# Kernel optimization log

Hardware: AMD Instinct MI355X
Metric: run time of the kernel (lower is better)

## Reference

```python
import jax, jax.numpy as jnp
import numpy as np

B, T, D, HD, HN, O = 32, 512, 512, 64, 16, 512
EPS = 1e-5


def setup_inputs() -> dict:
    key = jax.random.key(0)
    ks = jax.random.split(key, 12)
    s = lambda fan_in: 1.0 / np.sqrt(fan_in)
    inp = {
        "inputs": jax.random.normal(ks[0], (B, T, D), dtype=jnp.float32),
        "Wq": jax.random.uniform(ks[1], (HN, D, HD), jnp.float32, -s(D), s(D)),
        "bq": jnp.zeros((HN, HD), jnp.float32),
        "Wk": jax.random.uniform(ks[2], (HN, D, HD), jnp.float32, -s(D), s(D)),
        "bk": jnp.zeros((HN, HD), jnp.float32),
        "Wv": jax.random.uniform(ks[3], (HN, D, HD), jnp.float32, -s(D), s(D)),
        "bv": jnp.zeros((HN, HD), jnp.float32),
        "Wr": jax.random.uniform(ks[4], (D, O), jnp.float32, -s(D), s(D)),
        "br": jnp.zeros((O,), jnp.float32),
        "Wo": jax.random.uniform(ks[5], (HN * HD, O), jnp.float32, -s(HN * HD), s(HN * HD)),
        "bo": jnp.zeros((O,), jnp.float32),
        "ln1_w": jnp.ones((O,), jnp.float32),
        "ln1_b": jnp.zeros((O,), jnp.float32),
        "Wfc": jax.random.uniform(ks[6], (O, O), jnp.float32, -s(O), s(O)),
        "bfc": jnp.zeros((O,), jnp.float32),
        "ln2_w": jnp.ones((O,), jnp.float32),
        "ln2_b": jnp.zeros((O,), jnp.float32),
    }
    return inp


def _layernorm(x, w, b):
    mu = jnp.mean(x, axis=-1, keepdims=True)
    var = jnp.mean(jnp.square(x - mu), axis=-1, keepdims=True)
    return (x - mu) * jax.lax.rsqrt(var + EPS) * w + b


def reference(inputs, Wq, bq, Wk, bk, Wv, bv, Wr, br, Wo, bo,
              ln1_w, ln1_b, Wfc, bfc, ln2_w, ln2_b):
    # causal mask: multiply-then-subtract as in the original
    score_mask = jnp.tril(jnp.ones((T, T), jnp.float32))        # [T,T]
    padding_mask = (score_mask == 0).astype(jnp.float32) * 1e9  # [T,T]

    residual = inputs @ Wr + br                                  # [B,T,O]

    # batched per-head projections with nonstandard activations
    q = jax.nn.relu(jnp.einsum('btd,hdf->bhtf', inputs, Wq) + bq[None, :, None, :])
    k = jax.nn.relu(jnp.einsum('btd,hdf->bhtf', inputs, Wk) + bk[None, :, None, :])
    v = jnp.tanh(jnp.einsum('btd,hdf->bhtf', inputs, Wv) + bv[None, :, None, :])

    scores = jnp.einsum('bhtf,bhsf->bhts', q, k) / jnp.sqrt(jnp.float32(HD))
    scores = scores * score_mask - padding_mask                  # [B,H,T,T]
    weights = jax.nn.softmax(scores, axis=-1)
    heads = jnp.einsum('bhts,bhsf->bhtf', weights, v)            # [B,H,T,HD]

    # concat heads (head order preserved) + tanh output projection
    concat = heads.transpose(0, 2, 1, 3).reshape(B, T, HN * HD)
    out = jnp.tanh(concat @ Wo + bo)                             # [B,T,O]

    out = _layernorm(out + residual, ln1_w, ln1_b)
    fc = jax.nn.relu(out @ Wfc + bfc)
    out = _layernorm(fc + out, ln2_w, ln2_b)
    return out
```

## Files before the change

### kernel.cpp

```cpp
#include <hip/hip_runtime.h>
#include <hip/hip_bf16.h>

#define B_  32
#define T_  512
#define D_  512
#define HD_ 64
#define HN_ 16
#define O_  512
#define M_  (B_ * T_)
#define NQ_ (HN_ * HD_)

typedef __bf16 bf16;
typedef __attribute__((ext_vector_type(8))) __bf16 bf16x8;
typedef __attribute__((ext_vector_type(4))) __bf16 bf16x4;
typedef __attribute__((ext_vector_type(4))) float f32x4;

static __device__ __forceinline__ f32x4 mfma16(bf16x8 a, bf16x8 b, f32x4 c) {
    return __builtin_amdgcn_mfma_f32_16x16x32_bf16(a, b, c, 0, 0, 0);
}

static __device__ __forceinline__ void load_lds_16B(const bf16* g, bf16* l) {
    __builtin_amdgcn_global_load_lds(
        (const __attribute__((address_space(1))) unsigned int*)(unsigned long long)g,
        (__attribute__((address_space(3))) unsigned int*)(unsigned long long)l,
        16, 0, 0);
}

static __device__ __forceinline__ float fast_tanh(float x) {
    return 1.f - 2.f / (__expf(2.f * x) + 1.f);
}

static __device__ __forceinline__ int2 swz_block() {
    const int nx = gridDim.x;
    const int nwg = nx * gridDim.y;
    int l = blockIdx.y * nx + blockIdx.x;
    l = (l & 7) * (nwg >> 3) + (l >> 3);
    return make_int2(l % nx, l / nx);
}

__global__ __launch_bounds__(256) void prep_all_kernel(
    const float* __restrict__ inputs,
    const float* __restrict__ Wq, const float* __restrict__ Wk,
    const float* __restrict__ Wv, const float* __restrict__ Wr,
    const float* __restrict__ Wo, const float* __restrict__ Wfc,
    const float* __restrict__ bq, const float* __restrict__ bk,
    const float* __restrict__ bv, const float* __restrict__ br,
    bf16* __restrict__ xin, bf16* __restrict__ wall,
    bf16* __restrict__ wrt, bf16* __restrict__ wot, bf16* __restrict__ wfct,
    float* __restrict__ ball)
{
    __shared__ bf16 tl[64][72];
    const int tid = threadIdx.x;
    int id = blockIdx.x;

    if (id < 4096) {
        const size_t i = ((size_t)id * 256 + tid) * 8;
        f32x4 x0 = *(const f32x4*)(inputs + i);
        f32x4 x1 = *(const f32x4*)(inputs + i + 4);
        bf16x8 v;
        v[0] = (bf16)x0[0]; v[1] = (bf16)x0[1]; v[2] = (bf16)x0[2]; v[3] = (bf16)x0[3];
        v[4] = (bf16)x1[0]; v[5] = (bf16)x1[1]; v[6] = (bf16)x1[2]; v[7] = (bf16)x1[3];
        *(bf16x8*)(xin + i) = v;
        return;
    }
    if (id < 4480) {
        id -= 4096;
        const int kt = id & 7; id >>= 3;
        const int h = id & 15; id >>= 4;
        const float* src = (id == 0) ? Wq : (id == 1) ? Wk : Wv;
        bf16* dst = wall + (size_t)id * (1024 * 512);
        const int k0 = kt * 64;
#pragma unroll
        for (int i = 0; i < 4; i++) {
            const int e = i * 256 + tid;
            const int kk = e >> 4, f4 = (e & 15) * 4;
            const f32x4 v = *(const f32x4*)(src + ((size_t)h * 512 + k0 + kk) * 64 + f4);
#pragma unroll
            for (int j = 0; j < 4; j++) tl[f4 + j][kk] = (bf16)v[j];
        }
        __syncthreads();
#pragma unroll
        for (int i = 0; i < 2; i++) {
            const int e = i * 256 + tid;
            const int f = e >> 3, kc = (e & 7) * 8;
            *(bf16x8*)(dst + ((size_t)h * 64 + f) * 512 + k0 + kc) = *(const bf16x8*)&tl[f][kc];
        }
        return;
    }
    if (id < 4736) {
        id -= 4480;
        const float* src; bf16* dst; int K;
        if (id < 64)       { src = Wr;  dst = wrt;  K = 512;  }
        else if (id < 192) { src = Wo;  dst = wot;  K = 1024; id -= 64; }
        else               { src = Wfc; dst = wfct; K = 512;  id -= 192; }
        const int kt = id >> 3, nt = id & 7;
        const int k0 = kt * 64, n0 = nt * 64;
#pragma unroll
        for (int i = 0; i < 4; i++) {
            const int e = i * 256 + tid;
            const int kk = e >> 4, n4 = (e & 15) * 4;
            const f32x4 v = *(const f32x4*)(src + (size_t)(k0 + kk) * 512 + n0 + n4);
#pragma unroll
            for (int j = 0; j < 4; j++) tl[n4 + j][kk] = (bf16)v[j];
        }
        __syncthreads();
#pragma unroll
        for (int i = 0; i < 2; i++) {
            const int e = i * 256 + tid;
            const int nn = e >> 3, kc = (e & 7) * 8;
            *(bf16x8*)(dst + (size_t)(n0 + nn) * K + k0 + kc) = *(const bf16x8*)&tl[nn][kc];
        }
        return;
    }
    const int i = (id - 4736) * 256 + tid;
    float v = (i < 1024) ? bq[i]
            : (i < 2048) ? bk[i - 1024]
            : (i < 3072) ? bv[i - 2048] : br[i - 3072];
    ball[i] = v;
}

__global__ __launch_bounds__(512, 2) void gemm_qkvr256_kernel(
    const bf16* __restrict__ A, const bf16* __restrict__ Wall,
    const float* __restrict__ ball,
    bf16* __restrict__ qc, bf16* __restrict__ kb, bf16* __restrict__ vt,
    bf16* __restrict__ resb)
{
    __shared__ bf16 SL[65536];
    const int tid = threadIdx.x;
    const int lane = tid & 63;
    const int w = tid >> 6;
    const int wm = w >> 2, wn = w & 3;
    const int lr = lane & 15, lg = lane >> 4;
    const int K = 512;

    const int2 bc = swz_block();
    const int m0 = bc.y * 256, n0 = bc.x * 256;

    const int p = tid & 7;
    const int rr = tid >> 3;
    const int g = p ^ (rr & 7);
    const int arow0 = rr, arow1 = 128 + rr;
    const int brow0 = ((rr >> 5) << 6) | (rr & 31);
    const int brow1 = 128 + brow0;

    auto STAGE_H = [&](int t, int h) {
        const int slot = t & 1;
        const int k0 = t << 6;
        if ((h & 1) == 0) {
            bf16* Bb = SL + 32768 + slot * 16384;
            const int off = (h == 2) ? 32 : 0;
            const int r0_ = brow0 + off, r1_ = brow1 + off;
            load_lds_16B(Wall + (size_t)(n0 + r0_) * K + k0 + g * 8, Bb + r0_ * 64 + p * 8);
            load_lds_16B(Wall + (size_t)(n0 + r1_) * K + k0 + g * 8, Bb + r1_ * 64 + p * 8);
        } else {
            bf16* Ab = SL + slot * 16384;
            const int off = (h == 3) ? 64 : 0;
            const int r0_ = arow0 + off, r1_ = arow1 + off;
            load_lds_16B(A + (size_t)(m0 + r0_) * K + k0 + g * 8, Ab + r0_ * 64 + p * 8);
            load_lds_16B(A + (size_t)(m0 + r1_) * K + k0 + g * 8, Ab + r1_ * 64 + p * 8);
        }
    };

    const int x = lr & 7;
    auto LDA = [&](int t, int mi, int kc) -> bf16x8 {
        const int row = wm * 128 + mi * 16 + lr;
        const bf16* Ab = SL + (t & 1) * 16384;
        return *(const bf16x8*)&Ab[row * 64 + ((((kc << 2) | lg) ^ x) << 3)];
    };
    auto LDB = [&](int t, int nj, int kc) -> bf16x8 {
        const int row = wn * 64 + nj * 16 + lr;
        const bf16* Bb = SL + 32768 + (t & 1) * 16384;
        return *(const bf16x8*)&Bb[row * 64 + ((((kc << 2) | lg) ^ x) << 3)];
    };

    f32x4 acc[8][4];
    const f32x4 zero4 = {0.f, 0.f, 0.f, 0.f};
#pragma unroll
    for (int i = 0; i < 8; i++)
#pragma unroll
        for (int j = 0; j < 4; j++) acc[i][j] = zero4;

    bf16x8 b01[4], b23[4], af[8];

    STAGE_H(0, 0); STAGE_H(0, 1); STAGE_H(0, 2); STAGE_H(0, 3);

    for (int t = 0; t < 7; t++) {
        asm volatile("s_waitcnt vmcnt(4)\n\ts_barrier" ::: "memory");
#pragma unroll
        for (int nj = 0; nj < 2; nj++)
#pragma unroll
            for (int kc = 0; kc < 2; kc++) b01[nj * 2 + kc] = LDB(t, nj, kc);
#pragma unroll
        for (int mi = 0; mi < 4; mi++)
#pragma unroll
            for (int kc = 0; kc < 2; kc++) af[mi * 2 + kc] = LDA(t, mi, kc);
        STAGE_H(t + 1, 0);
        __builtin_amdgcn_s_setprio(1);
#pragma unroll
        for (int mi = 0; mi < 4; mi++)
#pragma unroll
            for (int nj = 0; nj < 2; nj++)
#pragma unroll
                for (int kc = 0; kc < 2; kc++)
                    acc[mi][nj] = mfma16(af[mi * 2 + kc], b01[nj * 2 + kc], acc[mi][nj]);
        __builtin_amdgcn_s_setprio(0);
        asm volatile("s_waitcnt vmcnt(4)\n\ts_barrier" ::: "memory");
#pragma unroll
        for (int nj = 0; nj < 2; nj++)
#pragma unroll
            for (int kc = 0; kc < 2; kc++) b23[nj * 2 + kc] = LDB(t, nj + 2, kc);
        STAGE_H(t + 1, 1);
        __builtin_amdgcn_s_setprio(1);
#pragma unroll
        for (int mi = 0; mi < 4; mi++)
#pragma unroll
            for (int nj = 0; nj < 2; nj++)
#pragma unroll
                for (int kc = 0; kc < 2; kc++)
                    acc[mi][nj + 2] = mfma16(af[mi * 2 + kc], b23[nj * 2 + kc], acc[mi][nj + 2]);
        __builtin_amdgcn_s_setprio(0);
        asm volatile("s_waitcnt vmcnt(4)\n\ts_barrier" ::: "memory");
#pragma unroll
        for (int mi = 0; mi < 4; mi++)
#pragma unroll
            for (int kc = 0; kc < 2; kc++) af[mi * 2 + kc] = LDA(t, mi + 4, kc);
        STAGE_H(t + 1, 2);
        __builtin_amdgcn_s_setprio(1);
#pragma unroll
        for (int mi = 0; mi < 4; mi++)
#pragma unroll
            for (int nj = 0; nj < 2; nj++)
#pragma unroll
                for (int kc = 0; kc < 2; kc++)
                    acc[mi + 4][nj] = mfma16(af[mi * 2 + kc], b01[nj * 2 + kc], acc[mi + 4][nj]);
        __builtin_amdgcn_s_setprio(0);
        STAGE_H(t + 1, 3);
        __builtin_amdgcn_s_setprio(1);
#pragma unroll
        for (int mi = 0; mi < 4; mi++)
#pragma unroll
            for (int nj = 0; nj < 2; nj++)
#pragma unroll
                for (int kc = 0; kc < 2; kc++)
                    acc[mi + 4][nj + 2] = mfma16(af[mi * 2 + kc], b23[nj * 2 + kc], acc[mi + 4][nj + 2]);
        __builtin_amdgcn_s_setprio(0);
    }

    {
        const int t = 7;
        asm volatile("s_waitcnt vmcnt(4)\n\ts_barrier" ::: "memory");
#pragma unroll
        for (int nj = 0; nj < 2; nj++)
#pragma unroll
            for (int kc = 0; kc < 2; kc++) b01[nj * 2 + kc] = LDB(t, nj, kc);
#pragma unroll
        for (int mi = 0; mi < 4; mi++)
#pragma unroll
            for (int kc = 0; kc < 2; kc++) af[mi * 2 + kc] = LDA(t, mi, kc);
        __builtin_amdgcn_s_setprio(1);
#pragma unroll
        for (int mi = 0; mi < 4; mi++)
#pragma unroll
            for (int nj = 0; nj < 2; nj++)
#pragma unroll
                for (int kc = 0; kc < 2; kc++)
                    acc[mi][nj] = mfma16(af[mi * 2 + kc], b01[nj * 2 + kc], acc[mi][nj]);
        __builtin_amdgcn_s_setprio(0);
        asm volatile("s_waitcnt vmcnt(2)\n\ts_barrier" ::: "memory");
#pragma unroll
        for (int nj = 0; nj < 2; nj++)
#pragma unroll
            for (int kc = 0; kc < 2; kc++) b23[nj * 2 + kc] = LDB(t, nj + 2, kc);
        __builtin_amdgcn_s_setprio(1);
#pragma unroll
        for (int mi = 0; mi < 4; mi++)
#pragma unroll
            for (int nj = 0; nj < 2; nj++)
#pragma unroll
                for (int kc = 0; kc < 2; kc++)
                    acc[mi][nj + 2] = mfma16(af[mi * 2 + kc], b23[nj * 2 + kc], acc[mi][nj + 2]);
        __builtin_amdgcn_s_setprio(0);
        asm volatile("s_waitcnt vmcnt(0)\n\ts_barrier" ::: "memory");
#pragma unroll
        for (int mi = 0; mi < 4; mi++)
#pragma unroll
            for (int kc = 0; kc < 2; kc++) af[mi * 2 + kc] = LDA(t, mi + 4, kc);
        __builtin_amdgcn_s_setprio(1);
#pragma unroll
        for (int mi = 0; mi < 4; mi++)
#pragma unroll
            for (int nj = 0; nj < 2; nj++)
#pragma unroll
                for (int kc = 0; kc < 2; kc++)
                    acc[mi + 4][nj] = mfma16(af[mi * 2 + kc], b01[nj * 2 + kc], acc[mi + 4][nj]);
#pragma unroll
        for (int mi = 0; mi < 4; mi++)
#pragma unroll
            for (int nj = 0; nj < 2; nj++)
#pragma unroll
                for (int kc = 0; kc < 2; kc++)
                    acc[mi + 4][nj + 2] = mfma16(af[mi * 2 + kc], b23[nj * 2 + kc], acc[mi + 4][nj + 2]);
        __builtin_amdgcn_s_setprio(0);
    }
    __syncthreads();

    const int region = n0 >> 10;
    if (region == 2) {
#pragma unroll
        for (int mi = 0; mi < 8; mi++) {
#pragma unroll
            for (int nj = 0; nj < 4; nj++) {
                const int n = n0 + wn * 64 + nj * 16 + lr;
                const float bn = ball[n];
                const int m = m0 + wm * 128 + mi * 16 + lg * 4;
                const int bb = m >> 9, tt = m & 511;
                const int nn = n - 2048, hh = nn >> 6, f = nn & 63;
                bf16x4 st;
#pragma unroll
                for (int r = 0; r < 4; r++) st[r] = (bf16)fast_tanh(acc[mi][nj][r] + bn);
                *(bf16x4*)(vt + (((size_t)(bb * 16 + hh) * 64 + f) << 9) + tt) = st;
            }
        }
    } else {
        bf16* dst; int pitch, nb; float scale = 1.f; bool rl = false;
        if (region == 0)      { dst = qc;   pitch = 1024; nb = n0;        scale = 0.125f; rl = true; }
        else if (region == 1) { dst = kb;   pitch = 1024; nb = n0 - 1024; rl = true; }
        else                  { dst = resb; pitch = 512;  nb = n0 - 3072; }
        float bn[4];
#pragma unroll
        for (int nj = 0; nj < 4; nj++) bn[nj] = ball[n0 + wn * 64 + nj * 16 + lr];
#pragma unroll
        for (int half = 0; half < 2; half++) {
            if (wm == half) {
#pragma unroll
                for (int mi = 0; mi < 8; mi++) {
#pragma unroll
                    for (int nj = 0; nj < 4; nj++) {
                        const int col = wn * 64 + nj * 16 + lr;
#pragma unroll
                        for (int r = 0; r < 4; r++) {
                            float v = acc[mi][nj][r] + bn[nj];
                            if (rl) v = fmaxf(v, 0.f);
                            SL[(mi * 16 + lg * 4 + r) * 264 + col] = (bf16)(v * scale);
                        }
                    }
                }
            }
            __syncthreads();
#pragma unroll
            for (int i = 0; i < 4; i++) {
                const int rr2 = i * 32 + (tid >> 4);
                const int cc = (tid & 15) * 16;
                bf16x8 v0 = *(const bf16x8*)&SL[rr2 * 264 + cc];
                bf16x8 v1 = *(const bf16x8*)&SL[rr2 * 264 + cc + 8];
                bf16* pdst = dst + (size_t)(m0 + half * 128 + rr2) * pitch + nb + cc;
                *(bf16x8*)pdst = v0;
                *(bf16x8*)(pdst + 8) = v1;
            }
            __syncthreads();
        }
    }
}

template <int ACT, bool F32OUT>
__global__ __launch_bounds__(512) void gemm_ln_kernel(
    const bf16* __restrict__ A, const bf16* __restrict__ Wt,
    const float* __restrict__ bias, const bf16* __restrict__ partner,
    const float* __restrict__ lnw, const float* __restrict__ lnb,
    void* __restrict__ outv, const int K)
{
    __shared__ bf16 SL[73728];
    __shared__ float parts[2][4][64];
    const int tid = threadIdx.x;
    const int lane = tid & 63;
    const int w = tid >> 6;
    const int wr = w >> 2, wn = w & 3;
    const int lr = lane & 15, lg = lane >> 4;
    const int m0 = blockIdx.x * 64;
    const int nt = K >> 5;

    const int gs = (tid & 3) ^ ((tid >> 3) & 3);
    const bf16* aP = A + (size_t)(m0 + (tid >> 2)) * K + gs * 8;
    const bf16* bP = Wt + (size_t)(tid >> 2) * K + gs * 8;

    auto STAGE = [&](int t) {
        bf16* Ab = SL + (t & 3) * 2048;
        bf16* Bb = SL + 8192 + (t & 3) * 16384;
        const int k0 = t << 5;
        if (tid < 256) load_lds_16B(aP + k0, Ab + tid * 8);
#pragma unroll
        for (int j = 0; j < 4; j++)
            load_lds_16B(bP + k0 + (size_t)(j * 128) * K, Bb + j * 4096 + tid * 8);
    };

    f32x4 acc[2][8];
    const f32x4 zero4 = {0.f, 0.f, 0.f, 0.f};
#pragma unroll
    for (int i = 0; i < 2; i++)
#pragma unroll
        for (int j = 0; j < 8; j++) acc[i][j] = zero4;

    STAGE(0); STAGE(1);
    if (w < 4) asm volatile("s_waitcnt vmcnt(5)" ::: "memory");
    else       asm volatile("s_waitcnt vmcnt(4)" ::: "memory");
    __builtin_amdgcn_s_barrier();

    for (int t = 0; t < nt; t++) {
        if (t + 2 < nt) {
            STAGE(t + 2);
            if (w < 4) asm volatile("s_waitcnt vmcnt(5)" ::: "memory");
            else       asm volatile("s_waitcnt vmcnt(4)" ::: "memory");
        } else {
            asm volatile("s_waitcnt vmcnt(0)" ::: "memory");
        }
        __builtin_amdgcn_s_barrier();

        const bf16* Ab = SL + (t & 3) * 2048;
        const bf16* Bb = SL + 8192 + (t & 3) * 16384;
        bf16x8 a[2], b[8];
#pragma unroll
        for (int mi = 0; mi < 2; mi++) {
            const int row = wr * 32 + mi * 16 + lr;
            a[mi] = *(const bf16x8*)&Ab[row * 32 + ((lg ^ ((row >> 1) & 3)) << 3)];
        }
#pragma unroll
        for (int nj = 0; nj < 8; nj++) {
            const int row = wn * 128 + nj * 16 + lr;
            b[nj] = *(const bf16x8*)&Bb[row * 32 + ((lg ^ ((row >> 1) & 3)) << 3)];
        }
        __builtin_amdgcn_s_setprio(1);
#pragma unroll
        for (int mi = 0; mi < 2; mi++)
#pragma unroll
            for (int nj = 0; nj < 8; nj++)
                acc[mi][nj] = mfma16(a[mi], b[nj], acc[mi][nj]);
        __builtin_amdgcn_s_setprio(0);
    }
    __syncthreads();

    bf16* SLp = SL;
#pragma unroll
    for (int jj = 0; jj < 8; jj++) {
        const int e = jj * 512 + tid;
        const int row = e >> 6, col = (e & 63) * 8;
        *(bf16x8*)&SLp[row * 520 + col] =
            *(const bf16x8*)(partner + (size_t)(m0 + row) * 512 + col);
    }
    __syncthreads();

    float bn[8], lw[8], lb[8];
#pragma unroll
    for (int nj = 0; nj < 8; nj++) {
        const int col = wn * 128 + nj * 16 + lr;
        bn[nj] = bias[col]; lw[nj] = lnw[col]; lb[nj] = lnb[col];
    }

    float rs[8], rq[8];
#pragma unroll
    for (int i = 0; i < 8; i++) { rs[i] = 0.f; rq[i] = 0.f; }
#pragma unroll
    for (int mi = 0; mi < 2; mi++)
#pragma unroll
        for (int r = 0; r < 4; r++) {
            const int row = wr * 32 + mi * 16 + lg * 4 + r;
            float ps = 0.f, pq = 0.f;
#pragma unroll
            for (int nj = 0; nj < 8; nj++) {
                float x = acc[mi][nj][r] + bn[nj];
                if constexpr (ACT == 1) x = fmaxf(x, 0.f);
                else if constexpr (ACT == 2) x = fast_tanh(x);
                x += (float)SLp[row * 520 + wn * 128 + nj * 16 + lr];
                acc[mi][nj][r] = x;
                ps += x; pq += x * x;
            }
            rs[mi * 4 + r] = ps; rq[mi * 4 + r] = pq;
        }
#pragma unroll
    for (int i = 0; i < 8; i++) {
#pragma unroll
        for (int off = 1; off <= 8; off <<= 1) {
            rs[i] += __shfl_xor(rs[i], off);
            rq[i] += __shfl_xor(rq[i], off);
        }
    }
    if (lr == 0) {
#pragma unroll
        for (int mi = 0; mi < 2; mi++)
#pragma unroll
            for (int r = 0; r < 4; r++) {
                const int row = wr * 32 + mi * 16 + lg * 4 + r;
                parts[0][wn][row] = rs[mi * 4 + r];
                parts[1][wn][row] = rq[mi * 4 + r];
            }
    }
    __syncthreads();

    float mean_[8], inv_[8];
#pragma unroll
    for (int mi = 0; mi < 2; mi++)
#pragma unroll
        for (int r = 0; r < 4; r++) {
            const int row = wr * 32 + mi * 16 + lg * 4 + r;
            const float S = parts[0][0][row] + parts[0][1][row] + parts[0][2][row] + parts[0][3][row];
            const float Q = parts[1][0][row] + parts[1][1][row] + parts[1][2][row] + parts[1][3][row];
            const float m = S * (1.f / 512.f);
            mean_[mi * 4 + r] = m;
            inv_[mi * 4 + r] = rsqrtf(Q * (1.f / 512.f) - m * m + 1e-5f);
        }

    if constexpr (F32OUT) {
        float* outp = (float*)outv;
#pragma unroll
        for (int mi = 0; mi < 2; mi++)
#pragma unroll
            for (int r = 0; r < 4; r++) {
                const int row = wr * 32 + mi * 16 + lg * 4 + r;
                const float m = mean_[mi * 4 + r], iv = inv_[mi * 4 + r];
#pragma unroll
                for (int nj = 0; nj < 8; nj++) {
                    const int col = wn * 128 + nj * 16 + lr;
                    outp[(size_t)(m0 + row) * 512 + col] =
                        (acc[mi][nj][r] - m) * iv * lw[nj] + lb[nj];
                }
            }
    } else {
        bf16* SLy = SL + 36864;
#pragma unroll
        for (int mi = 0; mi < 2; mi++)
#pragma unroll
            for (int r = 0; r < 4; r++) {
                const int row = wr * 32 + mi * 16 + lg * 4 + r;
                const float m = mean_[mi * 4 + r], iv = inv_[mi * 4 + r];
#pragma unroll
                for (int nj = 0; nj < 8; nj++) {
                    const int col = wn * 128 + nj * 16 + lr;
                    SLy[row * 520 + col] = (bf16)((acc[mi][nj][r] - m) * iv * lw[nj] + lb[nj]);
                }
            }
        __syncthreads();
        bf16* outp = (bf16*)outv;
#pragma unroll
        for (int jj = 0; jj < 8; jj++) {
            const int e = jj * 512 + tid;
            const int row = e >> 6, col = (e & 63) * 8;
            *(bf16x8*)(outp + (size_t)(m0 + row) * 512 + col) =
                *(const bf16x8*)&SLy[row * 520 + col];
        }
    }
}

static __device__ __forceinline__ int sigma_k(int t) {
    return (t & 32) | ((t & 4) << 2) | ((t & 24) >> 1) | (t & 3);
}

__global__ __launch_bounds__(256) void mfma_attn_kernel(
    const bf16* __restrict__ Kb, const bf16* __restrict__ Vt, bf16* __restrict__ QC)
{
    __shared__ bf16 Ks[2][64][72];
    __shared__ bf16 Vts[2][64][72];

    int l = blockIdx.x;
    l = (l & 7) * 256 + (l >> 3);
    const int qb = l & 3;
    const int h = (l >> 2) & 15;
    const int b = l >> 6;
    const int tid = threadIdx.x;
    const int lane = tid & 63;
    const int w = tid >> 6;
    const int lr = lane & 15, lg = lane >> 4;

    const int qrow0 = qb * 128 + w * 32;
    const size_t qbase = ((size_t)b * T_ + qrow0) * NQ_ + h * 64;
    const int bh = b * HN_ + h;

    bf16x8 qf[2][2];
#pragma unroll
    for (int mi = 0; mi < 2; mi++)
#pragma unroll
        for (int kc = 0; kc < 2; kc++)
            qf[mi][kc] = *(const bf16x8*)(QC + qbase + (size_t)(mi * 16 + lr) * NQ_ + kc * 32 + lg * 8);

    const f32x4 zero4 = {0.f, 0.f, 0.f, 0.f};
    f32x4 o[2][4];
    float m_st[2] = {-1e30f, -1e30f}, l_st[2] = {0.f, 0.f};
#pragma unroll
    for (int mi = 0; mi < 2; mi++)
#pragma unroll
        for (int dj = 0; dj < 4; dj++) o[mi][dj] = zero4;

    const int nsb = 2 * qb + 2;

    bf16x8 kreg[2], vreg[2];
    auto LOADR = [&](int sb) {
#pragma unroll
        for (int i = 0; i < 2; i++) {
            const int ci = i * 256 + tid, row = ci >> 3, cc = ci & 7;
            kreg[i] = *(const bf16x8*)(Kb + ((size_t)b * T_ + sb * 64 + row) * NQ_ + h * 64 + cc * 8);
            vreg[i] = *(const bf16x8*)(Vt + ((size_t)bh * 64 + row) * T_ + sb * 64 + cc * 8);
        }
    };
    auto WRITE = [&](int buf) {
#pragma unroll
        for (int i = 0; i < 2; i++) {
            const int ci = i * 256 + tid, row = ci >> 3, cc = ci & 7;
            *(bf16x8*)&Ks[buf][sigma_k(row)][cc * 8] = kreg[i];
            *(bf16x8*)&Vts[buf][row][cc * 8] = vreg[i];
        }
    };

    LOADR(0); WRITE(0); __syncthreads();
    int cur = 0;

    for (int sb = 0; sb < nsb; sb++) {
        const bool pf = (sb + 1 < nsb);
        if (pf) LOADR(sb + 1);

        if (sb * 64 <= qrow0 + 31) {
            f32x4 sc[2][4];
#pragma unroll
            for (int mi = 0; mi < 2; mi++)
#pragma unroll
                for (int nj = 0; nj < 4; nj++) sc[mi][nj] = zero4;
            __builtin_amdgcn_s_setprio(1);
#pragma unroll
            for (int kc = 0; kc < 2; kc++) {
                bf16x8 kf[4];
#pragma unroll
                for (int nj = 0; nj < 4; nj++)
                    kf[nj] = *(const bf16x8*)&Ks[cur][nj * 16 + lr][kc * 32 + lg * 8];
#pragma unroll
                for (int mi = 0; mi < 2; mi++)
#pragma unroll
                    for (int nj = 0; nj < 4; nj++)
                        sc[mi][nj] = mfma16(kf[nj], qf[mi][kc], sc[mi][nj]);
            }
            __builtin_amdgcn_s_setprio(0);
            const bool needmask = (sb * 64 + 63 > qrow0);
            float tm[2];
#pragma unroll
            for (int mi = 0; mi < 2; mi++) {
                const int qg = qrow0 + mi * 16 + lr;
                float mx = -1e30f;
#pragma unroll
                for (int nj = 0; nj < 4; nj++) {
                    const int kvb = sb * 64 + ((nj >> 1) << 5) + ((nj & 1) << 2) + lg * 8;
#pragma unroll
                    for (int r = 0; r < 4; r++) {
                        float s = sc[mi][nj][r];
                        if (needmask && (kvb + r > qg)) s = -1e30f;
                        sc[mi][nj][r] = s;
                        mx = fmaxf(mx, s);
                    }
                }
                mx = fmaxf(mx, __shfl_xor(mx, 16));
                mx = fmaxf(mx, __shfl_xor(mx, 32));
                tm[mi] = mx;
            }
            const bool defer = (tm[0] <= m_st[0] + 8.f) && (tm[1] <= m_st[1] + 8.f);
            if (!__all(defer)) {
#pragma unroll
                for (int mi = 0; mi < 2; mi++) {
                    const float mn = fmaxf(m_st[mi], tm[mi]);
                    const float sf = __expf(m_st[mi] - mn);
                    m_st[mi] = mn;
                    l_st[mi] *= sf;
#pragma unroll
                    for (int dj = 0; dj < 4; dj++)
#pragma unroll
                        for (int r = 0; r < 4; r++) o[mi][dj][r] *= sf;
                }
            }
            bf16x4 pk[2][4];
#pragma unroll
            for (int mi = 0; mi < 2; mi++) {
                float ts = 0.f;
#pragma unroll
                for (int nj = 0; nj < 4; nj++)
#pragma unroll
                    for (int r = 0; r < 4; r++) {
                        const float p2 = __expf(sc[mi][nj][r] - m_st[mi]);
                        ts += p2;
                        pk[mi][nj][r] = (bf16)p2;
                    }
                ts += __shfl_xor(ts, 16);
                ts += __shfl_xor(ts, 32);
                l_st[mi] += ts;
            }
            __builtin_amdgcn_s_setprio(1);
#pragma unroll
            for (int kc = 0; kc < 2; kc++) {
                bf16x8 vf[4], pf2[2];
#pragma unroll
                for (int mi = 0; mi < 2; mi++) {
                    bf16x8 t;
#pragma unroll
                    for (int r = 0; r < 4; r++) { t[r] = pk[mi][2 * kc][r]; t[r + 4] = pk[mi][2 * kc + 1][r]; }
                    pf2[mi] = t;
                }
#pragma unroll
                for (int dj = 0; dj < 4; dj++)
                    vf[dj] = *(const bf16x8*)&Vts[cur][dj * 16 + lr][kc * 32 + lg * 8];
#pragma unroll
                for (int mi = 0; mi < 2; mi++)
#pragma unroll
                    for (int dj = 0; dj < 4; dj++)
                        o[mi][dj] = mfma16(vf[dj], pf2[mi], o[mi][dj]);
            }
            __builtin_amdgcn_s_setprio(0);
        }

        if (pf) WRITE(cur ^ 1);
        __syncthreads();
        cur ^= 1;
    }

#pragma unroll
    for (int mi = 0; mi < 2; mi++) {
        const float inv = 1.f / l_st[mi];
        const size_t rowoff = qbase + (size_t)(mi * 16 + lr) * NQ_;
#pragma unroll
        for (int dj = 0; dj < 4; dj++) {
            bf16x4 st;
#pragma unroll
            for (int r = 0; r < 4; r++) st[r] = (bf16)(o[mi][dj][r] * inv);
            *(bf16x4*)(QC + rowoff + dj * 16 + lg * 4) = st;
        }
    }
}

extern "C" void kernel_launch(void* const* d_in, const int* in_sizes, int n_in,
                              void* d_out, int out_size, void* d_ws, size_t ws_size,
                              hipStream_t stream)
{
    const float* inputs = (const float*)d_in[0];
    const float* Wq = (const float*)d_in[1];
    const float* bq = (const float*)d_in[2];
    const float* Wk = (const float*)d_in[3];
    const float* bk = (const float*)d_in[4];
    const float* Wv = (const float*)d_in[5];
    const float* bv = (const float*)d_in[6];
    const float* Wr = (const float*)d_in[7];
    const float* br = (const float*)d_in[8];
    const float* Wo = (const float*)d_in[9];
    const float* bo = (const float*)d_in[10];
    const float* ln1w = (const float*)d_in[11];
    const float* ln1b = (const float*)d_in[12];
    const float* Wfc = (const float*)d_in[13];
    const float* bfc = (const float*)d_in[14];
    const float* ln2w = (const float*)d_in[15];
    const float* ln2b = (const float*)d_in[16];
    float* out = (float*)d_out;

    const size_t MB = 1024ull * 1024ull;
    char* ws = (char*)d_ws;
    bf16* qc   = (bf16*)(ws);
    bf16* kb   = (bf16*)(ws + 32 * MB);
    bf16* vt   = (bf16*)(ws + 64 * MB);
    bf16* xin  = (bf16*)(ws + 96 * MB);
    bf16* wall = (bf16*)(ws + 112 * MB);
    bf16* wot  = (bf16*)(ws + 112 * MB + 3670016);
    bf16* wfct = (bf16*)(ws + 112 * MB + 3670016 + 1048576);
    float* ball = (float*)(ws + 112 * MB + 3670016 + 1048576 + 524288);
    bf16* resb = (bf16*)d_out;
    bf16* ln1  = kb + (size_t)8 * MB;

    const dim3 blk(256);

    prep_all_kernel<<<dim3(4750), blk, 0, stream>>>(
        inputs, Wq, Wk, Wv, Wr, Wo, Wfc, bq, bk, bv, br,
        xin, wall, wall + (size_t)3072 * 512, wot, wfct, ball);

    gemm_qkvr256_kernel<<<dim3(14, 64), dim3(512), 0, stream>>>(
        xin, wall, ball, qc, kb, vt, resb);
    mfma_attn_kernel<<<dim3(B_ * HN_ * 4), blk, 0, stream>>>(kb, vt, qc);
    gemm_ln_kernel<2, false><<<dim3(256), dim3(512), 0, stream>>>(
        qc, wot, bo, resb, ln1w, ln1b, ln1, 1024);
    gemm_ln_kernel<1, true><<<dim3(256), dim3(512), 0, stream>>>(
        ln1, wfct, bfc, ln1, ln2w, ln2b, out, 512);
}
```

Before: 238.5 us.

## Restructure QKV GEMM mainloop to 4-stage K=32 LDS pipeline

Replaces the double-buffered K=64 staging with a four-slot ring of K=32 tiles in the fused QKV/residual GEMM, prefetching three steps ahead with a simpler A/B split and a new XOR swizzle. The aim is to hide global-to-LDS latency better and to simplify the per-step schedule. It also lowers the launch-bounds occupancy hint from 2 to 1 blocks per CU, which frees registers but may reduce latency hiding across blocks. The extra barriers per step and the smaller K per barrier add synchronization overhead.

```diff
diff --git a/kernel.cpp b/kernel.cpp
--- a/kernel.cpp
+++ b/kernel.cpp
@@ -119,7 +119,7 @@
     ball[i] = v;
 }
 
-__global__ __launch_bounds__(512, 2) void gemm_qkvr256_kernel(
+__global__ __launch_bounds__(512, 1) void gemm_qkvr256_kernel(
     const bf16* __restrict__ A, const bf16* __restrict__ Wall,
     const float* __restrict__ ball,
     bf16* __restrict__ qc, bf16* __restrict__ kb, bf16* __restrict__ vt,
@@ -136,41 +136,37 @@
     const int2 bc = swz_block();
     const int m0 = bc.y * 256, n0 = bc.x * 256;
 
-    const int p = tid & 7;
-    const int rr = tid >> 3;
-    const int g = p ^ (rr & 7);
-    const int arow0 = rr, arow1 = 128 + rr;
-    const int brow0 = ((rr >> 5) << 6) | (rr & 31);
-    const int brow1 = 128 + brow0;
-
-    auto STAGE_H = [&](int t, int h) {
-        const int slot = t & 1;
-        const int k0 = t << 6;
-        if ((h & 1) == 0) {
-            bf16* Bb = SL + 32768 + slot * 16384;
-            const int off = (h == 2) ? 32 : 0;
-            const int r0_ = brow0 + off, r1_ = brow1 + off;
-            load_lds_16B(Wall + (size_t)(n0 + r0_) * K + k0 + g * 8, Bb + r0_ * 64 + p * 8);
-            load_lds_16B(Wall + (size_t)(n0 + r1_) * K + k0 + g * 8, Bb + r1_ * 64 + p * 8);
-        } else {
-            bf16* Ab = SL + slot * 16384;
-            const int off = (h == 3) ? 64 : 0;
-            const int r0_ = arow0 + off, r1_ = arow1 + off;
-            load_lds_16B(A + (size_t)(m0 + r0_) * K + k0 + g * 8, Ab + r0_ * 64 + p * 8);
-            load_lds_16B(A + (size_t)(m0 + r1_) * K + k0 + g * 8, Ab + r1_ * 64 + p * 8);
-        }
+    const int c0r = tid >> 2, c0s = tid & 3;
+    const int g0 = c0s ^ ((c0r >> 1) & 3);
+    const int c1r = c0r + 128;
+    const int g1 = c0s ^ ((c1r >> 1) & 3);
+    const bf16* aP0 = A + (size_t)(m0 + c0r) * K + g0 * 8;
+    const bf16* aP1 = A + (size_t)(m0 + c1r) * K + g1 * 8;
+    const bf16* bP0 = Wall + (size_t)(n0 + c0r) * K + g0 * 8;
+    const bf16* bP1 = Wall + (size_t)(n0 + c1r) * K + g1 * 8;
+
+    auto STAGE_A = [&](int t) {
+        bf16* Ab = SL + (t & 3) * 8192;
+        const int k0 = t << 5;
+        load_lds_16B(aP0 + k0, Ab + tid * 8);
+        load_lds_16B(aP1 + k0, Ab + (tid + 512) * 8);
     };
-
-    const int x = lr & 7;
-    auto LDA = [&](int t, int mi, int kc) -> bf16x8 {
+    auto STAGE_B = [&](int t) {
+        bf16* Bb = SL + 32768 + (t & 3) * 8192;
+        const int k0 = t << 5;
+        load_lds_16B(bP0 + k0, Bb + tid * 8);
+        load_lds_16B(bP1 + k0, Bb + (tid + 512) * 8);
+    };
+
+    auto LDA = [&](int t, int mi) -> bf16x8 {
         const int row = wm * 128 + mi * 16 + lr;
-        const bf16* Ab = SL + (t & 1) * 16384;
-        return *(const bf16x8*)&Ab[row * 64 + ((((kc << 2) | lg) ^ x) << 3)];
+        const bf16* Ab = SL + (t & 3) * 8192;
+        return *(const bf16x8*)&Ab[row * 32 + ((lg ^ ((row >> 1) & 3)) << 3)];
     };
-    auto LDB = [&](int t, int nj, int kc) -> bf16x8 {
+    auto LDB = [&](int t, int nj) -> bf16x8 {
         const int row = wn * 64 + nj * 16 + lr;
-        const bf16* Bb = SL + 32768 + (t & 1) * 16384;
-        return *(const bf16x8*)&Bb[row * 64 + ((((kc << 2) | lg) ^ x) << 3)];
+        const bf16* Bb = SL + 32768 + (t & 3) * 8192;
+        return *(const bf16x8*)&Bb[row * 32 + ((lg ^ ((row >> 1) & 3)) << 3)];
     };
 
     f32x4 acc[8][4];
@@ -180,127 +176,40 @@
 #pragma unroll
         for (int j = 0; j < 4; j++) acc[i][j] = zero4;
 
-    bf16x8 b01[4], b23[4], af[8];
-
-    STAGE_H(0, 0); STAGE_H(0, 1); STAGE_H(0, 2); STAGE_H(0, 3);
-
-    for (int t = 0; t < 7; t++) {
-        asm volatile("s_waitcnt vmcnt(4)\n\ts_barrier" ::: "memory");
-#pragma unroll
-        for (int nj = 0; nj < 2; nj++)
-#pragma unroll
-            for (int kc = 0; kc < 2; kc++) b01[nj * 2 + kc] = LDB(t, nj, kc);
+    STAGE_A(0); STAGE_B(0); STAGE_A(1); STAGE_B(1); STAGE_A(2); STAGE_B(2);
+    asm volatile("s_waitcnt vmcnt(8)\n\ts_barrier" ::: "memory");
+
+    for (int t = 0; t < 16; t++) {
+        bf16x8 b[4], a[4];
+#pragma unroll
+        for (int nj = 0; nj < 4; nj++) b[nj] = LDB(t, nj);
+#pragma unroll
+        for (int mi = 0; mi < 4; mi++) a[mi] = LDA(t, mi);
+        if (t + 3 < 16) STAGE_A(t + 3);
+        asm volatile("s_barrier" ::: "memory");
+        __builtin_amdgcn_s_setprio(1);
 #pragma unroll
         for (int mi = 0; mi < 4; mi++)
 #pragma unroll
-            for (int kc = 0; kc < 2; kc++) af[mi * 2 + kc] = LDA(t, mi, kc);
-        STAGE_H(t + 1, 0);
+            for (int nj = 0; nj < 4; nj++)
+                acc[mi][nj] = mfma16(a[mi], b[nj], acc[mi][nj]);
+        __builtin_amdgcn_s_setprio(0);
+        asm volatile("s_barrier" ::: "memory");
+#pragma unroll
+        for (int mi = 0; mi < 4; mi++) a[mi] = LDA(t, mi + 4);
+        if (t + 3 < 16) STAGE_B(t + 3);
+        asm volatile("s_barrier" ::: "memory");
         __builtin_amdgcn_s_setprio(1);
 #pragma unroll
         for (int mi = 0; mi < 4; mi++)
 #pragma unroll
-            for (int nj = 0; nj < 2; nj++)
-#pragma unroll
-                for (int kc = 0; kc < 2; kc++)
-                    acc[mi][nj] = mfma16(af[mi * 2 + kc], b01[nj * 2 + kc], acc[mi][nj]);
+            for (int nj = 0; nj < 4; nj++)
+                acc[mi + 4][nj] = mfma16(a[mi], b[nj], acc[mi + 4][nj]);
         __builtin_amdgcn_s_setprio(0);
-        asm volatile("s_waitcnt vmcnt(4)\n\ts_barrier" ::: "memory");
-#pragma unroll
-        for (int nj = 0; nj < 2; nj++)
-#pragma unroll
-            for (int kc = 0; kc < 2; kc++) b23[nj * 2 + kc] = LDB(t, nj + 2, kc);
-        STAGE_H(t + 1, 1);
-        __builtin_amdgcn_s_setprio(1);
-#pragma unroll
-        for (int mi = 0; mi < 4; mi++)
-#pragma unroll
-            for (int nj = 0; nj < 2; nj++)
-#pragma unroll
-                for (int kc = 0; kc < 2; kc++)
-                    acc[mi][nj + 2] = mfma16(af[mi * 2 + kc], b23[nj * 2 + kc], acc[mi][nj + 2]);
-        __builtin_amdgcn_s_setprio(0);
-        asm volatile("s_waitcnt vmcnt(4)\n\ts_barrier" ::: "memory");
-#pragma unroll
-        for (int mi = 0; mi < 4; mi++)
-#pragma unroll
-            for (int kc = 0; kc < 2; kc++) af[mi * 2 + kc] = LDA(t, mi + 4, kc);
-        STAGE_H(t + 1, 2);
-        __builtin_amdgcn_s_setprio(1);
-#pragma unroll
-        for (int mi = 0; mi < 4; mi++)
-#pragma unroll
-            for (int nj = 0; nj < 2; nj++)
-#pragma unroll
-                for (int kc = 0; kc < 2; kc++)
-                    acc[mi + 4][nj] = mfma16(af[mi * 2 + kc], b01[nj * 2 + kc], acc[mi + 4][nj]);
-        __builtin_amdgcn_s_setprio(0);
-        STAGE_H(t + 1, 3);
-        __builtin_amdgcn_s_setprio(1);
-#pragma unroll
-        for (int mi = 0; mi < 4; mi++)
-#pragma unroll
-            for (int nj = 0; nj < 2; nj++)
-#pragma unroll
-                for (int kc = 0; kc < 2; kc++)
-                    acc[mi + 4][nj + 2] = mfma16(af[mi * 2 + kc], b23[nj * 2 + kc], acc[mi + 4][nj + 2]);
-        __builtin_amdgcn_s_setprio(0);
-    }
-
-    {
-        const int t = 7;
-        asm volatile("s_waitcnt vmcnt(4)\n\ts_barrier" ::: "memory");
-#pragma unroll
-        for (int nj = 0; nj < 2; nj++)
-#pragma unroll
-            for (int kc = 0; kc < 2; kc++) b01[nj * 2 + kc] = LDB(t, nj, kc);
-#pragma unroll
-        for (int mi = 0; mi < 4; mi++)
-#pragma unroll
-            for (int kc = 0; kc < 2; kc++) af[mi * 2 + kc] = LDA(t, mi, kc);
-        __builtin_amdgcn_s_setprio(1);
-#pragma unroll
-        for (int mi = 0; mi < 4; mi++)
-#pragma unroll
-            for (int nj = 0; nj < 2; nj++)
-#pragma unroll
-                for (int kc = 0; kc < 2; kc++)
-                    acc[mi][nj] = mfma16(af[mi * 2 + kc], b01[nj * 2 + kc], acc[mi][nj]);
-        __builtin_amdgcn_s_setprio(0);
-        asm volatile("s_waitcnt vmcnt(2)\n\ts_barrier" ::: "memory");
-#pragma unroll
-        for (int nj = 0; nj < 2; nj++)
-#pragma unroll
-            for (int kc = 0; kc < 2; kc++) b23[nj * 2 + kc] = LDB(t, nj + 2, kc);
-        __builtin_amdgcn_s_setprio(1);
-#pragma unroll
-        for (int mi = 0; mi < 4; mi++)
-#pragma unroll
-            for (int nj = 0; nj < 2; nj++)
-#pragma unroll
-                for (int kc = 0; kc < 2; kc++)
-                    acc[mi][nj + 2] = mfma16(af[mi * 2 + kc], b23[nj * 2 + kc], acc[mi][nj + 2]);
-        __builtin_amdgcn_s_setprio(0);
-        asm volatile("s_waitcnt vmcnt(0)\n\ts_barrier" ::: "memory");
-#pragma unroll
-        for (int mi = 0; mi < 4; mi++)
-#pragma unroll
-            for (int kc = 0; kc < 2; kc++) af[mi * 2 + kc] = LDA(t, mi + 4, kc);
-        __builtin_amdgcn_s_setprio(1);
-#pragma unroll
-        for (int mi = 0; mi < 4; mi++)
-#pragma unroll
-            for (int nj = 0; nj < 2; nj++)
-#pragma unroll
-                for (int kc = 0; kc < 2; kc++)
-                    acc[mi + 4][nj] = mfma16(af[mi * 2 + kc], b01[nj * 2 + kc], acc[mi + 4][nj]);
-#pragma unroll
-        for (int mi = 0; mi < 4; mi++)
-#pragma unroll
-            for (int nj = 0; nj < 2; nj++)
-#pragma unroll
-                for (int kc = 0; kc < 2; kc++)
-                    acc[mi + 4][nj + 2] = mfma16(af[mi * 2 + kc], b23[nj * 2 + kc], acc[mi + 4][nj + 2]);
-        __builtin_amdgcn_s_setprio(0);
+        if (t <= 12)      asm volatile("s_waitcnt vmcnt(8)" ::: "memory");
+        else if (t == 13) asm volatile("s_waitcnt vmcnt(4)" ::: "memory");
+        else if (t == 14) asm volatile("s_waitcnt vmcnt(0)" ::: "memory");
+        asm volatile("s_barrier" ::: "memory");
     }
     __syncthreads();
 
```

After: 245.1 us. 1.03x slower.

## Fuse output projection LN1 and FC LN2 into one kernel with fp32 residual

Applied to the files above, without the earlier changes.

Merges the two gemm+layernorm kernels into one, so the LN1 result stays in shared memory and feeds the FC GEMM directly instead of round-tripping through global memory. The FC weights are read straight from global memory per k-step without LDS staging or pipelining. The residual projection is now written as fp32 into the output buffer with uncoalesced scalar stores, then read back and rounded to bf16. This removes a launch and an intermediate buffer, but the second GEMM may stall on unstaged global loads and the residual traffic doubles in size.

```diff
diff --git a/kernel.cpp b/kernel.cpp
--- a/kernel.cpp
+++ b/kernel.cpp
@@ -123,7 +123,7 @@
     const bf16* __restrict__ A, const bf16* __restrict__ Wall,
     const float* __restrict__ ball,
     bf16* __restrict__ qc, bf16* __restrict__ kb, bf16* __restrict__ vt,
-    bf16* __restrict__ resb)
+    float* __restrict__ resf)
 {
     __shared__ bf16 SL[65536];
     const int tid = threadIdx.x;
@@ -321,11 +321,25 @@
                 *(bf16x4*)(vt + (((size_t)(bb * 16 + hh) * 64 + f) << 9) + tt) = st;
             }
         }
+    } else if (region == 3) {
+#pragma unroll
+        for (int mi = 0; mi < 8; mi++) {
+#pragma unroll
+            for (int nj = 0; nj < 4; nj++) {
+                const int n = n0 + wn * 64 + nj * 16 + lr;
+                const float bn = ball[n];
+                const int nn = n - 3072;
+#pragma unroll
+                for (int r = 0; r < 4; r++) {
+                    const int m = m0 + wm * 128 + mi * 16 + lg * 4 + r;
+                    resf[(size_t)m * 512 + nn] = acc[mi][nj][r] + bn;
+                }
+            }
+        }
     } else {
-        bf16* dst; int pitch, nb; float scale = 1.f; bool rl = false;
-        if (region == 0)      { dst = qc;   pitch = 1024; nb = n0;        scale = 0.125f; rl = true; }
-        else if (region == 1) { dst = kb;   pitch = 1024; nb = n0 - 1024; rl = true; }
-        else                  { dst = resb; pitch = 512;  nb = n0 - 3072; }
+        bf16* dst; int nb; float scale = 1.f;
+        if (region == 0) { dst = qc; nb = n0;        scale = 0.125f; }
+        else             { dst = kb; nb = n0 - 1024; }
         float bn[4];
 #pragma unroll
         for (int nj = 0; nj < 4; nj++) bn[nj] = ball[n0 + wn * 64 + nj * 16 + lr];
@@ -339,8 +353,7 @@
                         const int col = wn * 64 + nj * 16 + lr;
 #pragma unroll
                         for (int r = 0; r < 4; r++) {
-                            float v = acc[mi][nj][r] + bn[nj];
-                            if (rl) v = fmaxf(v, 0.f);
+                            float v = fmaxf(acc[mi][nj][r] + bn[nj], 0.f);
                             SL[(mi * 16 + lg * 4 + r) * 264 + col] = (bf16)(v * scale);
                         }
                     }
@@ -353,7 +366,7 @@
                 const int cc = (tid & 15) * 16;
                 bf16x8 v0 = *(const bf16x8*)&SL[rr2 * 264 + cc];
                 bf16x8 v1 = *(const bf16x8*)&SL[rr2 * 264 + cc + 8];
-                bf16* pdst = dst + (size_t)(m0 + half * 128 + rr2) * pitch + nb + cc;
+                bf16* pdst = dst + (size_t)(m0 + half * 128 + rr2) * 1024 + nb + cc;
                 *(bf16x8*)pdst = v0;
                 *(bf16x8*)(pdst + 8) = v1;
             }
@@ -362,26 +375,29 @@
     }
 }
 
-template <int ACT, bool F32OUT>
-__global__ __launch_bounds__(512) void gemm_ln_kernel(
-    const bf16* __restrict__ A, const bf16* __restrict__ Wt,
-    const float* __restrict__ bias, const bf16* __restrict__ partner,
-    const float* __restrict__ lnw, const float* __restrict__ lnb,
-    void* __restrict__ outv, const int K)
+__global__ __launch_bounds__(512) void gemm_ln_fused_kernel(
+    const bf16* __restrict__ qc, const bf16* __restrict__ wot,
+    const float* __restrict__ bo, const float* resf,
+    const float* __restrict__ ln1w, const float* __restrict__ ln1b,
+    const bf16* __restrict__ wfct, const float* __restrict__ bfc,
+    const float* __restrict__ ln2w, const float* __restrict__ ln2b,
+    float* outp)
 {
     __shared__ bf16 SL[73728];
     __shared__ float parts[2][4][64];
+    bf16* SLp = SL;
+    bf16* SLy = SL + 36864;
     const int tid = threadIdx.x;
     const int lane = tid & 63;
     const int w = tid >> 6;
     const int wr = w >> 2, wn = w & 3;
     const int lr = lane & 15, lg = lane >> 4;
     const int m0 = blockIdx.x * 64;
-    const int nt = K >> 5;
+    const int K1 = 1024;
 
     const int gs = (tid & 3) ^ ((tid >> 3) & 3);
-    const bf16* aP = A + (size_t)(m0 + (tid >> 2)) * K + gs * 8;
-    const bf16* bP = Wt + (size_t)(tid >> 2) * K + gs * 8;
+    const bf16* aP = qc + (size_t)(m0 + (tid >> 2)) * K1 + gs * 8;
+    const bf16* bP = wot + (size_t)(tid >> 2) * K1 + gs * 8;
 
     auto STAGE = [&](int t) {
         bf16* Ab = SL + (t & 3) * 2048;
@@ -390,7 +406,7 @@
         if (tid < 256) load_lds_16B(aP + k0, Ab + tid * 8);
 #pragma unroll
         for (int j = 0; j < 4; j++)
-            load_lds_16B(bP + k0 + (size_t)(j * 128) * K, Bb + j * 4096 + tid * 8);
+            load_lds_16B(bP + k0 + (size_t)(j * 128) * K1, Bb + j * 4096 + tid * 8);
     };
 
     f32x4 acc[2][8];
@@ -405,8 +421,8 @@
     else       asm volatile("s_waitcnt vmcnt(4)" ::: "memory");
     __builtin_amdgcn_s_barrier();
 
-    for (int t = 0; t < nt; t++) {
-        if (t + 2 < nt) {
+    for (int t = 0; t < 32; t++) {
+        if (t + 2 < 32) {
             STAGE(t + 2);
             if (w < 4) asm volatile("s_waitcnt vmcnt(5)" ::: "memory");
             else       asm volatile("s_waitcnt vmcnt(4)" ::: "memory");
@@ -438,26 +454,27 @@
     }
     __syncthreads();
 
-    bf16* SLp = SL;
 #pragma unroll
     for (int jj = 0; jj < 8; jj++) {
         const int e = jj * 512 + tid;
         const int row = e >> 6, col = (e & 63) * 8;
-        *(bf16x8*)&SLp[row * 520 + col] =
-            *(const bf16x8*)(partner + (size_t)(m0 + row) * 512 + col);
+        const f32x4 u0 = *(const f32x4*)(resf + (size_t)(m0 + row) * 512 + col);
+        const f32x4 u1 = *(const f32x4*)(resf + (size_t)(m0 + row) * 512 + col + 4);
+        bf16x8 v;
+#pragma unroll
+        for (int q = 0; q < 4; q++) { v[q] = (bf16)u0[q]; v[4 + q] = (bf16)u1[q]; }
+        *(bf16x8*)&SLp[row * 520 + col] = v;
     }
     __syncthreads();
 
-    float bn[8], lw[8], lb[8];
+    float lw[8], lb[8], bn[8];
 #pragma unroll
     for (int nj = 0; nj < 8; nj++) {
         const int col = wn * 128 + nj * 16 + lr;
-        bn[nj] = bias[col]; lw[nj] = lnw[col]; lb[nj] = lnb[col];
+        bn[nj] = bo[col]; lw[nj] = ln1w[col]; lb[nj] = ln1b[col];
     }
 
     float rs[8], rq[8];
-#pragma unroll
-    for (int i = 0; i < 8; i++) { rs[i] = 0.f; rq[i] = 0.f; }
 #pragma unroll
     for (int mi = 0; mi < 2; mi++)
 #pragma unroll
@@ -466,12 +483,10 @@
             float ps = 0.f, pq = 0.f;
 #pragma unroll
             for (int nj = 0; nj < 8; nj++) {
-                float x = acc[mi][nj][r] + bn[nj];
-                if constexpr (ACT == 1) x = fmaxf(x, 0.f);
-                else if constexpr (ACT == 2) x = fast_tanh(x);
-                x += (float)SLp[row * 520 + wn * 128 + nj * 16 + lr];
-                acc[mi][nj][r] = x;
-                ps += x; pq += x * x;
+                float xv = fast_tanh(acc[mi][nj][r] + bn[nj]);
+                xv += (float)SLp[row * 520 + wn * 128 + nj * 16 + lr];
+                acc[mi][nj][r] = xv;
+                ps += xv; pq += xv * xv;
             }
             rs[mi * 4 + r] = ps; rq[mi * 4 + r] = pq;
         }
@@ -495,7 +510,6 @@
     }
     __syncthreads();
 
-    float mean_[8], inv_[8];
 #pragma unroll
     for (int mi = 0; mi < 2; mi++)
 #pragma unroll
@@ -503,50 +517,96 @@
             const int row = wr * 32 + mi * 16 + lg * 4 + r;
             const float S = parts[0][0][row] + parts[0][1][row] + parts[0][2][row] + parts[0][3][row];
             const float Q = parts[1][0][row] + parts[1][1][row] + parts[1][2][row] + parts[1][3][row];
-            const float m = S * (1.f / 512.f);
-            mean_[mi * 4 + r] = m;
-            inv_[mi * 4 + r] = rsqrtf(Q * (1.f / 512.f) - m * m + 1e-5f);
-        }
-
-    if constexpr (F32OUT) {
-        float* outp = (float*)outv;
+            const float mm = S * (1.f / 512.f);
+            const float iv = rsqrtf(Q * (1.f / 512.f) - mm * mm + 1e-5f);
+#pragma unroll
+            for (int nj = 0; nj < 8; nj++) {
+                const int col = wn * 128 + nj * 16 + lr;
+                SLy[row * 520 + col] = (bf16)((acc[mi][nj][r] - mm) * iv * lw[nj] + lb[nj]);
+            }
+        }
+    __syncthreads();
+
+#pragma unroll
+    for (int i = 0; i < 2; i++)
+#pragma unroll
+        for (int j = 0; j < 8; j++) acc[i][j] = zero4;
+
+    for (int t2 = 0; t2 < 16; t2++) {
+        bf16x8 a2[2], b2[8];
+#pragma unroll
+        for (int nj = 0; nj < 8; nj++)
+            b2[nj] = *(const bf16x8*)(wfct + (size_t)(wn * 128 + nj * 16 + lr) * 512 + t2 * 32 + lg * 8);
+#pragma unroll
+        for (int mi = 0; mi < 2; mi++)
+            a2[mi] = *(const bf16x8*)&SLy[(wr * 32 + mi * 16 + lr) * 520 + t2 * 32 + lg * 8];
+        __builtin_amdgcn_s_setprio(1);
+#pragma unroll
+        for (int mi = 0; mi < 2; mi++)
+#pragma unroll
+            for (int nj = 0; nj < 8; nj++)
+                acc[mi][nj] = mfma16(a2[mi], b2[nj], acc[mi][nj]);
+        __builtin_amdgcn_s_setprio(0);
+    }
+
+#pragma unroll
+    for (int nj = 0; nj < 8; nj++) {
+        const int col = wn * 128 + nj * 16 + lr;
+        bn[nj] = bfc[col]; lw[nj] = ln2w[col]; lb[nj] = ln2b[col];
+    }
+
+#pragma unroll
+    for (int mi = 0; mi < 2; mi++)
+#pragma unroll
+        for (int r = 0; r < 4; r++) {
+            const int row = wr * 32 + mi * 16 + lg * 4 + r;
+            float ps = 0.f, pq = 0.f;
+#pragma unroll
+            for (int nj = 0; nj < 8; nj++) {
+                float xv = fmaxf(acc[mi][nj][r] + bn[nj], 0.f);
+                xv += (float)SLy[row * 520 + wn * 128 + nj * 16 + lr];
+                acc[mi][nj][r] = xv;
+                ps += xv; pq += xv * xv;
+            }
+            rs[mi * 4 + r] = ps; rq[mi * 4 + r] = pq;
+        }
+#pragma unroll
+    for (int i = 0; i < 8; i++) {
+#pragma unroll
+        for (int off = 1; off <= 8; off <<= 1) {
+            rs[i] += __shfl_xor(rs[i], off);
+            rq[i] += __shfl_xor(rq[i], off);
+        }
+    }
+    __syncthreads();
+    if (lr == 0) {
 #pragma unroll
         for (int mi = 0; mi < 2; mi++)
 #pragma unroll
             for (int r = 0; r < 4; r++) {
                 const int row = wr * 32 + mi * 16 + lg * 4 + r;
-                const float m = mean_[mi * 4 + r], iv = inv_[mi * 4 + r];
-#pragma unroll
-                for (int nj = 0; nj < 8; nj++) {
-                    const int col = wn * 128 + nj * 16 + lr;
-                    outp[(size_t)(m0 + row) * 512 + col] =
-                        (acc[mi][nj][r] - m) * iv * lw[nj] + lb[nj];
-                }
-            }
-    } else {
-        bf16* SLy = SL + 36864;
-#pragma unroll
-        for (int mi = 0; mi < 2; mi++)
-#pragma unroll
-            for (int r = 0; r < 4; r++) {
-                const int row = wr * 32 + mi * 16 + lg * 4 + r;
-                const float m = mean_[mi * 4 + r], iv = inv_[mi * 4 + r];
-#pragma unroll
-                for (int nj = 0; nj < 8; nj++) {
-                    const int col = wn * 128 + nj * 16 + lr;
-                    SLy[row * 520 + col] = (bf16)((acc[mi][nj][r] - m) * iv * lw[nj] + lb[nj]);
-                }
-            }
-        __syncthreads();
-        bf16* outp = (bf16*)outv;
-#pragma unroll
-        for (int jj = 0; jj < 8; jj++) {
-            const int e = jj * 512 + tid;
-            const int row = e >> 6, col = (e & 63) * 8;
-            *(bf16x8*)(outp + (size_t)(m0 + row) * 512 + col) =
-                *(const bf16x8*)&SLy[row * 520 + col];
-        }
-    }
+                parts[0][wn][row] = rs[mi * 4 + r];
+                parts[1][wn][row] = rq[mi * 4 + r];
+            }
+    }
+    __syncthreads();
+
+#pragma unroll
+    for (int mi = 0; mi < 2; mi++)
+#pragma unroll
+        for (int r = 0; r < 4; r++) {
+            const int row = wr * 32 + mi * 16 + lg * 4 + r;
+            const float S = parts[0][0][row] + parts[0][1][row] + parts[0][2][row] + parts[0][3][row];
+            const float Q = parts[1][0][row] + parts[1][1][row] + parts[1][2][row] + parts[1][3][row];
+            const float mm = S * (1.f / 512.f);
+            const float iv = rsqrtf(Q * (1.f / 512.f) - mm * mm + 1e-5f);
+#pragma unroll
+            for (int nj = 0; nj < 8; nj++) {
+                const int col = wn * 128 + nj * 16 + lr;
+                outp[(size_t)(m0 + row) * 512 + col] =
+                    (acc[mi][nj][r] - mm) * iv * lw[nj] + lb[nj];
+            }
+        }
 }
 
 static __device__ __forceinline__ int sigma_k(int t) {
@@ -761,8 +821,7 @@
     bf16* wot  = (bf16*)(ws + 112 * MB + 3670016);
     bf16* wfct = (bf16*)(ws + 112 * MB + 3670016 + 1048576);
     float* ball = (float*)(ws + 112 * MB + 3670016 + 1048576 + 524288);
-    bf16* resb = (bf16*)d_out;
-    bf16* ln1  = kb + (size_t)8 * MB;
+    float* resf = out;
 
     const dim3 blk(256);
 
@@ -771,10 +830,8 @@
         xin, wall, wall + (size_t)3072 * 512, wot, wfct, ball);
 
     gemm_qkvr256_kernel<<<dim3(14, 64), dim3(512), 0, stream>>>(
-        xin, wall, ball, qc, kb, vt, resb);
+        xin, wall, ball, qc, kb, vt, resf);
     mfma_attn_kernel<<<dim3(B_ * HN_ * 4), blk, 0, stream>>>(kb, vt, qc);
-    gemm_ln_kernel<2, false><<<dim3(256), dim3(512), 0, stream>>>(
-        qc, wot, bo, resb, ln1w, ln1b, ln1, 1024);
-    gemm_ln_kernel<1, true><<<dim3(256), dim3(512), 0, stream>>>(
-        ln1, wfct, bfc, ln1, ln2w, ln2b, out, 512);
-}
+    gemm_ln_fused_kernel<<<dim3(256), dim3(512), 0, stream>>>(
+        qc, wot, bo, resf, ln1w, ln1b, wfct, bfc, ln2w, ln2b, out);
+}
```

Measured after the change: 241.8 us. Within noise of the previous version (+1.4%).
